# Kernel optimization log

Measured on AMD Instinct MI355X. Metric: run time of the kernel, lower is better.

The kernel has to match this reference:

```python
import jax, jax.numpy as jnp
import numpy as np

N, M, D, H = 256, 1024, 512, 512


def setup_inputs() -> dict:
    key = jax.random.key(0)
    k1, k2, k3, k4 = jax.random.split(key, 4)
    scale = 1.0 / np.sqrt(D)
    return {
        "embeddings": jax.random.normal(k1, (N, D), dtype=jnp.float32),
        "support_tensors": jax.random.normal(k2, (M, D), dtype=jnp.float32),
        "W1": jax.random.normal(k3, (D, H), dtype=jnp.float32) * scale,
        "b1": jnp.zeros((H,), dtype=jnp.float32),
        "W2": jax.random.normal(k4, (H, 1), dtype=jnp.float32) * (1.0 / np.sqrt(H)),
        "b2": jnp.zeros((1,), dtype=jnp.float32),
    }


def reference(embeddings, support_tensors, W1, b1, W2, b2):
    # SupportLayer.call: tile queries x support set into all N*M pairs,
    # apply pairwise kernel (siamese head: sigmoid(MLP(|a - b|))),
    # reshape back to similarity matrix [N, M].
    # Broadcasting replaces the explicit tf.tile / reshape.
    diff = jnp.abs(embeddings[:, None, :] - support_tensors[None, :, :])  # [N, M, D]
    h = jax.nn.relu(jnp.einsum("nmd,dh->nmh", diff, W1) + b1)             # [N, M, H]
    logits = jnp.einsum("nmh,ho->nmo", h, W2)[..., 0] + b2[0]             # [N, M]
    return jax.nn.sigmoid(logits)
```

## Files before the change

### kernel.cpp

```cpp
#include <hip/hip_runtime.h>
#include <hip/hip_bf16.h>

#define N_Q 256
#define M_S 1024
#define DD 512
#define HH 512

typedef __attribute__((ext_vector_type(8))) short short8;
typedef __attribute__((ext_vector_type(8))) __bf16 bf16x8;
typedef __attribute__((ext_vector_type(16))) float f32x16;
typedef __attribute__((ext_vector_type(2))) __bf16 bf16x2;

union U8 { short8 s; bf16x8 b; };

__device__ __forceinline__ unsigned short f2bf(float f) {
  unsigned int u = __float_as_uint(f);
  u += 0x7FFFu + ((u >> 16) & 1u);
  return (unsigned short)(u >> 16);
}

__device__ __forceinline__ short8 pack8(const float* d) {
#if defined(__has_builtin) && __has_builtin(__builtin_amdgcn_cvt_pk_bf16_f32)
  short8 r;
#pragma unroll
  for (int i = 0; i < 4; ++i) {
    union { bf16x2 v; short s[2]; } u;
    u.v = __builtin_amdgcn_cvt_pk_bf16_f32(d[2 * i], d[2 * i + 1]);
    r[2 * i] = u.s[0];
    r[2 * i + 1] = u.s[1];
  }
  return r;
#else
  short8 r;
#pragma unroll
  for (int i = 0; i < 8; ++i) r[i] = (short)f2bf(d[i]);
  return r;
#endif
}

__device__ __forceinline__ short8 packdiff(float4 e0, float4 e1, float4 s0, float4 s1) {
  float d[8];
  d[0] = fabsf(e0.x - s0.x); d[1] = fabsf(e0.y - s0.y);
  d[2] = fabsf(e0.z - s0.z); d[3] = fabsf(e0.w - s0.w);
  d[4] = fabsf(e1.x - s1.x); d[5] = fabsf(e1.y - s1.y);
  d[6] = fabsf(e1.z - s1.z); d[7] = fabsf(e1.w - s1.w);
  return pack8(d);
}

__global__ __launch_bounds__(1024) void prep_w1s(const float* __restrict__ W1,
                                                 unsigned short* __restrict__ w1s) {
  const int gid = blockIdx.x * 1024 + threadIdx.x;
  const int k = gid >> 7;
  const int hq = gid & 127;
  const float4 w = *(const float4*)(W1 + k * HH + hq * 4);
  const int f = (k >> 4) * 16 + (hq >> 3);
  const int lk = ((k >> 3) & 1) * 32 + (hq & 7) * 4;
  const int j = k & 7;
  unsigned short* p = w1s + f * 512 + lk * 8 + j;
  p[0]  = f2bf(w.x);
  p[8]  = f2bf(w.y);
  p[16] = f2bf(w.z);
  p[24] = f2bf(w.w);
}

__global__ __launch_bounds__(512, 2) void support_kernel(
    const float* __restrict__ emb, const float* __restrict__ sup,
    const unsigned short* __restrict__ w1s, const float* __restrict__ b1,
    const float* __restrict__ W2, const float* __restrict__ b2,
    float* __restrict__ out) {
  extern __shared__ short8 As16[];

  const int tid = threadIdx.x;
  const int lane = tid & 63;
  const int wid = tid >> 6;
  const int l31 = lane & 31;
  const int khalf = lane >> 5;

  const int m0 = blockIdx.x * 16;
  const int n0 = blockIdx.y * 8;

  const unsigned short* bb = w1s + (wid * 2) * 512 + lane * 8;
  U8 b[4][2];
#pragma unroll
  for (int s = 0; s < 3; ++s)
#pragma unroll
    for (int tj = 0; tj < 2; ++tj)
      b[s][tj].s = *(const short8*)(bb + (s * 16 + tj) * 512);

  {
    const int c = tid & 63;
    const int rg = tid >> 6;
    const float* ep = emb + (n0 + rg) * DD + c * 8;
    const float4 e0 = *(const float4*)ep;
    const float4 e1 = *(const float4*)(ep + 4);
    const float* sbase = sup + m0 * DD + c * 8;
#pragma unroll
    for (int j = 0; j < 16; ++j) {
      const float4 s0 = *(const float4*)(sbase + j * DD);
      const float4 s1 = *(const float4*)(sbase + j * DD + 4);
      const int p = rg * 16 + j;
      As16[p * 64 + (c ^ (j & 7))] = packdiff(e0, e1, s0, s1);
    }
  }
  __syncthreads();

  const int ax = l31 & 7;
  const int ar0 = (0 * 32 + l31) * 64;
  const int ar1 = (1 * 32 + l31) * 64;
  const int ar2 = (2 * 32 + l31) * 64;
  const int ar3 = (3 * 32 + l31) * 64;

  f32x16 acc[4][2] = {};
  U8 a[3][4];
#pragma unroll
  for (int s = 0; s < 2; ++s) {
    const int c = (s * 2 + khalf) ^ ax;
    a[s][0].s = As16[ar0 + c];
    a[s][1].s = As16[ar1 + c];
    a[s][2].s = As16[ar2 + c];
    a[s][3].s = As16[ar3 + c];
  }

#pragma unroll
  for (int ks = 0; ks < 32; ++ks) {
    __builtin_amdgcn_s_setprio(1);
#pragma unroll
    for (int am = 0; am < 4; ++am)
#pragma unroll
      for (int tj = 0; tj < 2; ++tj)
        acc[am][tj] = __builtin_amdgcn_mfma_f32_32x32x16_bf16(
            b[ks & 3][tj].b, a[ks % 3][am].b, acc[am][tj], 0, 0, 0);
    __builtin_amdgcn_s_setprio(0);
    if (ks + 2 < 32) {
      const int cc = ((ks + 2) * 2 + khalf) ^ ax;
      const int slot = (ks + 2) % 3;
      a[slot][0].s = As16[ar0 + cc];
      a[slot][1].s = As16[ar1 + cc];
      a[slot][2].s = As16[ar2 + cc];
      a[slot][3].s = As16[ar3 + cc];
    }
    if (ks + 3 < 32) {
#pragma unroll
      for (int tj = 0; tj < 2; ++tj)
        b[(ks + 3) & 3][tj].s = *(const short8*)(bb + ((ks + 3) * 16 + tj) * 512);
    }
  }

  float s0a, s1a, s2a, s3a;
  {
    float sm[4] = {0.f, 0.f, 0.f, 0.f};
#pragma unroll
    for (int tj = 0; tj < 2; ++tj) {
      const float* b1p = b1 + (wid * 2 + tj) * 32 + khalf * 4;
      const float* w2p = W2 + (wid * 2 + tj) * 32 + khalf * 4;
#pragma unroll
      for (int rq = 0; rq < 4; ++rq) {
        const float4 b1q = *(const float4*)(b1p + rq * 8);
        const float4 w2q = *(const float4*)(w2p + rq * 8);
#pragma unroll
        for (int am = 0; am < 4; ++am) {
          sm[am] += fmaxf(acc[am][tj][rq * 4 + 0] + b1q.x, 0.f) * w2q.x;
          sm[am] += fmaxf(acc[am][tj][rq * 4 + 1] + b1q.y, 0.f) * w2q.y;
          sm[am] += fmaxf(acc[am][tj][rq * 4 + 2] + b1q.z, 0.f) * w2q.z;
          sm[am] += fmaxf(acc[am][tj][rq * 4 + 3] + b1q.w, 0.f) * w2q.w;
        }
      }
    }
#pragma unroll
    for (int am = 0; am < 4; ++am) sm[am] += __shfl_xor(sm[am], 32, 64);
    s0a = sm[0]; s1a = sm[1]; s2a = sm[2]; s3a = sm[3];
  }
  float* psums = (float*)(As16 + 128 * 64);
  {
    const float v0 = khalf ? s2a : s0a;
    const float v1 = khalf ? s3a : s1a;
    const int p0 = khalf * 64 + l31;
    psums[p0 * 9 + wid] = v0;
    psums[(p0 + 32) * 9 + wid] = v1;
  }
  __syncthreads();
  if (tid < 128) {
    float t = b2[0];
#pragma unroll
    for (int w = 0; w < 8; ++w) t += psums[tid * 9 + w];
    out[(n0 + (tid >> 4)) * M_S + m0 + (tid & 15)] = 1.f / (1.f + __expf(-t));
  }
}

extern "C" void kernel_launch(void* const* d_in, const int* in_sizes, int n_in,
                              void* d_out, int out_size, void* d_ws, size_t ws_size,
                              hipStream_t stream) {
  const float* emb = (const float*)d_in[0];
  const float* sup = (const float*)d_in[1];
  const float* W1  = (const float*)d_in[2];
  const float* b1  = (const float*)d_in[3];
  const float* W2  = (const float*)d_in[4];
  const float* b2  = (const float*)d_in[5];
  float* out = (float*)d_out;
  unsigned short* w1s = (unsigned short*)d_ws;

  static bool attr_done = false;
  if (!attr_done) {
    hipFuncSetAttribute((const void*)support_kernel,
                        hipFuncAttributeMaxDynamicSharedMemorySize, 135680);
    attr_done = true;
  }

  prep_w1s<<<64, 1024, 0, stream>>>(W1, w1s);
  support_kernel<<<dim3(M_S / 16, N_Q / 8), 512, 135680, stream>>>(
      emb, sup, w1s, b1, W2, b2, out);
}
```

Measured before the change: 192.0 us.

## Overlap second half of diff-tile construction with early MFMA iterations

The kernel no longer builds the whole bf16 |e-s| A tile before the main loop. Before the first barrier it builds only the first 256 feature columns. Each thread then writes the upper 256 columns during the first 8 MFMA iterations, double-buffering its support-row loads in registers. A mid-loop barrier at ks==13 makes those writes visible before the loop first reads them. This hides global-load and pack latency of the prologue behind matrix work, at the cost of extra registers, an extra block-wide barrier, and interleaved LDS writes competing with LDS reads.

```diff
diff --git a/kernel.cpp b/kernel.cpp
--- a/kernel.cpp
+++ b/kernel.cpp
@@ -79,6 +79,13 @@
   const int m0 = blockIdx.x * 16;
   const int n0 = blockIdx.y * 8;
 
+  const int c5 = tid & 31;
+  const int rh = tid >> 5;
+  const int erow = rh >> 1;
+  const int srow0 = (rh & 1) * 8;
+  const int cA = c5;
+  const int cB = c5 + 32;
+
   const unsigned short* bb = w1s + (wid * 2) * 512 + lane * 8;
   U8 b[4][2];
 #pragma unroll
@@ -87,19 +94,26 @@
     for (int tj = 0; tj < 2; ++tj)
       b[s][tj].s = *(const short8*)(bb + (s * 16 + tj) * 512);
 
+  const float* epB = emb + (n0 + erow) * DD + cB * 8;
+  const float4 e0B = *(const float4*)epB;
+  const float4 e1B = *(const float4*)(epB + 4);
+  const float* sbB = sup + (m0 + srow0) * DD + cB * 8;
+  float4 srng[2][2];
+  srng[0][0] = *(const float4*)(sbB + 0 * DD);
+  srng[0][1] = *(const float4*)(sbB + 0 * DD + 4);
+  srng[1][0] = *(const float4*)(sbB + 1 * DD);
+  srng[1][1] = *(const float4*)(sbB + 1 * DD + 4);
+
   {
-    const int c = tid & 63;
-    const int rg = tid >> 6;
-    const float* ep = emb + (n0 + rg) * DD + c * 8;
-    const float4 e0 = *(const float4*)ep;
-    const float4 e1 = *(const float4*)(ep + 4);
-    const float* sbase = sup + m0 * DD + c * 8;
-#pragma unroll
-    for (int j = 0; j < 16; ++j) {
-      const float4 s0 = *(const float4*)(sbase + j * DD);
-      const float4 s1 = *(const float4*)(sbase + j * DD + 4);
-      const int p = rg * 16 + j;
-      As16[p * 64 + (c ^ (j & 7))] = packdiff(e0, e1, s0, s1);
+    const float* epA = emb + (n0 + erow) * DD + cA * 8;
+    const float4 e0A = *(const float4*)epA;
+    const float4 e1A = *(const float4*)(epA + 4);
+    const float* sbA = sup + (m0 + srow0) * DD + cA * 8;
+#pragma unroll
+    for (int j = 0; j < 8; ++j) {
+      const float4 s0 = *(const float4*)(sbA + j * DD);
+      const float4 s1 = *(const float4*)(sbA + j * DD + 4);
+      As16[(rh * 8 + j) * 64 + (cA ^ j)] = packdiff(e0A, e1A, s0, s1);
     }
   }
   __syncthreads();
@@ -131,6 +145,14 @@
         acc[am][tj] = __builtin_amdgcn_mfma_f32_32x32x16_bf16(
             b[ks & 3][tj].b, a[ks % 3][am].b, acc[am][tj], 0, 0, 0);
     __builtin_amdgcn_s_setprio(0);
+    if (ks < 8) {
+      As16[(rh * 8 + ks) * 64 + (cB ^ ks)] =
+          packdiff(e0B, e1B, srng[ks & 1][0], srng[ks & 1][1]);
+      if (ks + 2 < 8) {
+        srng[ks & 1][0] = *(const float4*)(sbB + (ks + 2) * DD);
+        srng[ks & 1][1] = *(const float4*)(sbB + (ks + 2) * DD + 4);
+      }
+    }
     if (ks + 2 < 32) {
       const int cc = ((ks + 2) * 2 + khalf) ^ ax;
       const int slot = (ks + 2) % 3;
@@ -144,6 +166,7 @@
       for (int tj = 0; tj < 2; ++tj)
         b[(ks + 3) & 3][tj].s = *(const short8*)(bb + ((ks + 3) * 16 + tj) * 512);
     }
+    if (ks == 13) __syncthreads();
   }
 
   float s0a, s1a, s2a, s3a;
```

Measured after the change: 194.3 us. About the same (+1.2%).

## Stage W1 tiles into LDS via direct global-to-LDS loads with double buffering

Applied to the files above, without the earlier changes.

Replaces the per-wave register prefetch of W1 from global memory with global_load_lds DMA into a double-buffered LDS region. Each wave then reads its B fragments from LDS one step ahead, with explicit vmcnt waits. It also widens the A-tile XOR swizzle from 8 to 16 columns to cut LDS bank conflicts, and reuses the A region for the partial sums behind an extra barrier. LDS use rises to 160 KB, which limits occupancy to one block per CU. The code also relies on vmcnt ordering without a barrier between waves, but each wave only reads its own slice, so that should be safe.

```diff
diff --git a/kernel.cpp b/kernel.cpp
--- a/kernel.cpp
+++ b/kernel.cpp
@@ -68,7 +68,9 @@
     const unsigned short* __restrict__ w1s, const float* __restrict__ b1,
     const float* __restrict__ W2, const float* __restrict__ b2,
     float* __restrict__ out) {
-  extern __shared__ short8 As16[];
+  extern __shared__ char lds[];
+  short8* As16 = (short8*)lds;
+  char* wbuf = lds + 131072;
 
   const int tid = threadIdx.x;
   const int lane = tid & 63;
@@ -79,13 +81,19 @@
   const int m0 = blockIdx.x * 16;
   const int n0 = blockIdx.y * 8;
 
-  const unsigned short* bb = w1s + (wid * 2) * 512 + lane * 8;
-  U8 b[4][2];
-#pragma unroll
-  for (int s = 0; s < 3; ++s)
-#pragma unroll
-    for (int tj = 0; tj < 2; ++tj)
-      b[s][tj].s = *(const short8*)(bb + (s * 16 + tj) * 512);
+  const char* gW = (const char*)w1s + (wid * 2) * 1024 + lane * 16;
+  const int wslice = wid * 2048;
+
+#define STAGE_W1(KS) do {                                                     \
+    const char* _g = gW + (KS) * 16384;                                       \
+    char* _l = wbuf + (((KS) & 1) * 16384 + wslice);                          \
+    __builtin_amdgcn_global_load_lds(                                         \
+        (const __attribute__((address_space(1))) unsigned int*)(_g),          \
+        (__attribute__((address_space(3))) unsigned int*)(_l), 16, 0, 0);     \
+    __builtin_amdgcn_global_load_lds(                                         \
+        (const __attribute__((address_space(1))) unsigned int*)(_g + 1024),   \
+        (__attribute__((address_space(3))) unsigned int*)(_l + 1024), 16, 0, 0); \
+  } while (0)
 
   {
     const int c = tid & 63;
@@ -98,13 +106,14 @@
     for (int j = 0; j < 16; ++j) {
       const float4 s0 = *(const float4*)(sbase + j * DD);
       const float4 s1 = *(const float4*)(sbase + j * DD + 4);
-      const int p = rg * 16 + j;
-      As16[p * 64 + (c ^ (j & 7))] = packdiff(e0, e1, s0, s1);
-    }
-  }
+      As16[(rg * 16 + j) * 64 + (c ^ j)] = packdiff(e0, e1, s0, s1);
+    }
+  }
+  STAGE_W1(0);
+  STAGE_W1(1);
   __syncthreads();
 
-  const int ax = l31 & 7;
+  const int ax = l31 & 15;
   const int ar0 = (0 * 32 + l31) * 64;
   const int ar1 = (1 * 32 + l31) * 64;
   const int ar2 = (2 * 32 + l31) * 64;
@@ -120,6 +129,12 @@
     a[s][2].s = As16[ar2 + c];
     a[s][3].s = As16[ar3 + c];
   }
+  U8 bw[2][2];
+  {
+    const short8* wp = (const short8*)(wbuf + wslice);
+    bw[0][0].s = wp[lane];
+    bw[0][1].s = wp[64 + lane];
+  }
 
 #pragma unroll
   for (int ks = 0; ks < 32; ++ks) {
@@ -129,8 +144,20 @@
 #pragma unroll
       for (int tj = 0; tj < 2; ++tj)
         acc[am][tj] = __builtin_amdgcn_mfma_f32_32x32x16_bf16(
-            b[ks & 3][tj].b, a[ks % 3][am].b, acc[am][tj], 0, 0, 0);
+            bw[ks & 1][tj].b, a[ks % 3][am].b, acc[am][tj], 0, 0, 0);
     __builtin_amdgcn_s_setprio(0);
+    if (ks + 2 < 32) {
+      STAGE_W1(ks + 2);
+      asm volatile("s_waitcnt vmcnt(2)" ::: "memory");
+    } else if (ks == 30) {
+      asm volatile("s_waitcnt vmcnt(0)" ::: "memory");
+    }
+    if (ks + 1 < 32) {
+      const short8* wp =
+          (const short8*)(wbuf + (((ks + 1) & 1) * 16384 + wslice));
+      bw[(ks + 1) & 1][0].s = wp[lane];
+      bw[(ks + 1) & 1][1].s = wp[64 + lane];
+    }
     if (ks + 2 < 32) {
       const int cc = ((ks + 2) * 2 + khalf) ^ ax;
       const int slot = (ks + 2) % 3;
@@ -139,12 +166,8 @@
       a[slot][2].s = As16[ar2 + cc];
       a[slot][3].s = As16[ar3 + cc];
     }
-    if (ks + 3 < 32) {
-#pragma unroll
-      for (int tj = 0; tj < 2; ++tj)
-        b[(ks + 3) & 3][tj].s = *(const short8*)(bb + ((ks + 3) * 16 + tj) * 512);
-    }
-  }
+  }
+#undef STAGE_W1
 
   float s0a, s1a, s2a, s3a;
   {
@@ -170,7 +193,8 @@
     for (int am = 0; am < 4; ++am) sm[am] += __shfl_xor(sm[am], 32, 64);
     s0a = sm[0]; s1a = sm[1]; s2a = sm[2]; s3a = sm[3];
   }
-  float* psums = (float*)(As16 + 128 * 64);
+  __syncthreads();
+  float* psums = (float*)As16;
   {
     const float v0 = khalf ? s2a : s0a;
     const float v1 = khalf ? s3a : s1a;
@@ -202,11 +226,11 @@
   static bool attr_done = false;
   if (!attr_done) {
     hipFuncSetAttribute((const void*)support_kernel,
-                        hipFuncAttributeMaxDynamicSharedMemorySize, 135680);
+                        hipFuncAttributeMaxDynamicSharedMemorySize, 163840);
     attr_done = true;
   }
 
   prep_w1s<<<64, 1024, 0, stream>>>(W1, w1s);
-  support_kernel<<<dim3(M_S / 16, N_Q / 8), 512, 135680, stream>>>(
+  support_kernel<<<dim3(M_S / 16, N_Q / 8), 512, 163840, stream>>>(
       emb, sup, w1s, b1, W2, b2, out);
 }
```

Measured after the change: 195.5 us. No clear change (+1.8%).

## Hand-schedule LDS and global operand loads with inline asm and explicit waitcnts

Applied to the files above, without the earlier changes.

Replaces compiler-generated LDS reads of the A operand and global loads of the W1 B operand with inline-asm ds_read_b128 and global_load_dwordx4. Both use double-buffered register slots and explicit lgkmcnt/vmcnt waits with sched_barriers, so prefetches stay in flight across the MFMA block. The LDS swizzle also widens from an XOR over 8 chunks to 16, to cut bank conflicts. This gives exact control over the latency hiding, but it shortens the B prefetch depth from three stages to two and relies on correct manual waitcnt accounting.

```diff
diff --git a/kernel.cpp b/kernel.cpp
--- a/kernel.cpp
+++ b/kernel.cpp
@@ -10,8 +10,9 @@
 typedef __attribute__((ext_vector_type(8))) __bf16 bf16x8;
 typedef __attribute__((ext_vector_type(16))) float f32x16;
 typedef __attribute__((ext_vector_type(2))) __bf16 bf16x2;
-
-union U8 { short8 s; bf16x8 b; };
+typedef __attribute__((ext_vector_type(4))) int i32x4;
+
+union U8 { short8 s; bf16x8 b; i32x4 i; };
 
 __device__ __forceinline__ unsigned short f2bf(float f) {
   unsigned int u = __float_as_uint(f);
@@ -68,7 +69,9 @@
     const unsigned short* __restrict__ w1s, const float* __restrict__ b1,
     const float* __restrict__ W2, const float* __restrict__ b2,
     float* __restrict__ out) {
-  extern __shared__ short8 As16[];
+  extern __shared__ char lds[];
+  short8* As16 = (short8*)lds;
+  float* psums = (float*)(lds + 131072);
 
   const int tid = threadIdx.x;
   const int lane = tid & 63;
@@ -78,14 +81,6 @@
 
   const int m0 = blockIdx.x * 16;
   const int n0 = blockIdx.y * 8;
-
-  const unsigned short* bb = w1s + (wid * 2) * 512 + lane * 8;
-  U8 b[4][2];
-#pragma unroll
-  for (int s = 0; s < 3; ++s)
-#pragma unroll
-    for (int tj = 0; tj < 2; ++tj)
-      b[s][tj].s = *(const short8*)(bb + (s * 16 + tj) * 512);
 
   {
     const int c = tid & 63;
@@ -98,53 +93,69 @@
     for (int j = 0; j < 16; ++j) {
       const float4 s0 = *(const float4*)(sbase + j * DD);
       const float4 s1 = *(const float4*)(sbase + j * DD + 4);
-      const int p = rg * 16 + j;
-      As16[p * 64 + (c ^ (j & 7))] = packdiff(e0, e1, s0, s1);
+      As16[(rg * 16 + j) * 64 + (c ^ j)] = packdiff(e0, e1, s0, s1);
     }
   }
   __syncthreads();
 
-  const int ax = l31 & 7;
-  const int ar0 = (0 * 32 + l31) * 64;
-  const int ar1 = (1 * 32 + l31) * 64;
-  const int ar2 = (2 * 32 + l31) * 64;
-  const int ar3 = (3 * 32 + l31) * 64;
+  const int ax = l31 & 15;
+  const unsigned aB0 = (unsigned)(uintptr_t)(As16 + (0 * 32 + l31) * 64);
+  const unsigned aB1 = (unsigned)(uintptr_t)(As16 + (1 * 32 + l31) * 64);
+  const unsigned aB2 = (unsigned)(uintptr_t)(As16 + (2 * 32 + l31) * 64);
+  const unsigned aB3 = (unsigned)(uintptr_t)(As16 + (3 * 32 + l31) * 64);
+  const unsigned vbase = (unsigned)(wid * 2048 + lane * 16);
 
   f32x16 acc[4][2] = {};
-  U8 a[3][4];
-#pragma unroll
-  for (int s = 0; s < 2; ++s) {
-    const int c = (s * 2 + khalf) ^ ax;
-    a[s][0].s = As16[ar0 + c];
-    a[s][1].s = As16[ar1 + c];
-    a[s][2].s = As16[ar2 + c];
-    a[s][3].s = As16[ar3 + c];
-  }
+  U8 a[2][4], b[2][2];
+
+#define A_ISSUE(SLOT, PH) do {                                                \
+    const unsigned _x = (((unsigned)(2 * (PH) + khalf)) ^ (unsigned)ax) << 4; \
+    asm volatile("ds_read_b128 %0, %1" : "=v"(a[SLOT][0].i) : "v"(aB0 + _x)); \
+    asm volatile("ds_read_b128 %0, %1" : "=v"(a[SLOT][1].i) : "v"(aB1 + _x)); \
+    asm volatile("ds_read_b128 %0, %1" : "=v"(a[SLOT][2].i) : "v"(aB2 + _x)); \
+    asm volatile("ds_read_b128 %0, %1" : "=v"(a[SLOT][3].i) : "v"(aB3 + _x)); \
+  } while (0)
+#define B_ISSUE(SLOT, PH) do {                                                \
+    const unsigned _vo = vbase + (unsigned)(PH) * 16384u;                     \
+    asm volatile("global_load_dwordx4 %0, %1, %2"                             \
+                 : "=v"(b[SLOT][0].i) : "v"(_vo), "s"(w1s) : "memory");       \
+    asm volatile("global_load_dwordx4 %0, %1, %2 offset:1024"                 \
+                 : "=v"(b[SLOT][1].i) : "v"(_vo), "s"(w1s) : "memory");       \
+  } while (0)
+
+  A_ISSUE(0, 0);
+  A_ISSUE(1, 1);
+  B_ISSUE(0, 0);
+  B_ISSUE(1, 1);
 
 #pragma unroll
   for (int ks = 0; ks < 32; ++ks) {
+    if (ks < 31) {
+      asm volatile("s_waitcnt lgkmcnt(4)" ::: "memory");
+      __builtin_amdgcn_sched_barrier(0);
+      asm volatile("s_waitcnt vmcnt(2)" ::: "memory");
+      __builtin_amdgcn_sched_barrier(0);
+    } else {
+      asm volatile("s_waitcnt lgkmcnt(0)" ::: "memory");
+      __builtin_amdgcn_sched_barrier(0);
+      asm volatile("s_waitcnt vmcnt(0)" ::: "memory");
+      __builtin_amdgcn_sched_barrier(0);
+    }
     __builtin_amdgcn_s_setprio(1);
 #pragma unroll
     for (int am = 0; am < 4; ++am)
 #pragma unroll
       for (int tj = 0; tj < 2; ++tj)
         acc[am][tj] = __builtin_amdgcn_mfma_f32_32x32x16_bf16(
-            b[ks & 3][tj].b, a[ks % 3][am].b, acc[am][tj], 0, 0, 0);
+            b[ks & 1][tj].b, a[ks & 1][am].b, acc[am][tj], 0, 0, 0);
     __builtin_amdgcn_s_setprio(0);
     if (ks + 2 < 32) {
-      const int cc = ((ks + 2) * 2 + khalf) ^ ax;
-      const int slot = (ks + 2) % 3;
-      a[slot][0].s = As16[ar0 + cc];
-      a[slot][1].s = As16[ar1 + cc];
-      a[slot][2].s = As16[ar2 + cc];
-      a[slot][3].s = As16[ar3 + cc];
-    }
-    if (ks + 3 < 32) {
-#pragma unroll
-      for (int tj = 0; tj < 2; ++tj)
-        b[(ks + 3) & 3][tj].s = *(const short8*)(bb + ((ks + 3) * 16 + tj) * 512);
-    }
-  }
+      A_ISSUE(ks & 1, ks + 2);
+      B_ISSUE(ks & 1, ks + 2);
+    }
+  }
+#undef A_ISSUE
+#undef B_ISSUE
 
   float s0a, s1a, s2a, s3a;
   {
@@ -170,7 +181,6 @@
     for (int am = 0; am < 4; ++am) sm[am] += __shfl_xor(sm[am], 32, 64);
     s0a = sm[0]; s1a = sm[1]; s2a = sm[2]; s3a = sm[3];
   }
-  float* psums = (float*)(As16 + 128 * 64);
   {
     const float v0 = khalf ? s2a : s0a;
     const float v1 = khalf ? s3a : s1a;
@@ -182,7 +192,7 @@
   if (tid < 128) {
     float t = b2[0];
 #pragma unroll
-    for (int w = 0; w < 8; ++w) t += psums[tid * 9 + w];
+    for (int w8 = 0; w8 < 8; ++w8) t += psums[tid * 9 + w8];
     out[(n0 + (tid >> 4)) * M_S + m0 + (tid & 15)] = 1.f / (1.f + __expf(-t));
   }
 }
```

Result: no change. 190.3 us (-0.9%).
